# Optimization experiments

Hardware: AMD Instinct MI355X
Metric: run time of the kernel (lower is better)

## Reference

```python
import jax, jax.numpy as jnp
import numpy as np

N_NODES = 50000
N_EDGES = 800000
HDIM = 256
NUMRELS = 16


def setup_inputs() -> dict:
    key = jax.random.key(0)
    ks = jax.random.split(key, 9)
    h = jax.random.normal(ks[0], (N_NODES, HDIM), dtype=jnp.float32)
    relvectors = jax.random.normal(ks[1], (NUMRELS, HDIM), dtype=jnp.float32)
    # GRUCell params (torch layout: [3*hdim, hdim] rows = [r, z, n])
    s = 1.0 / np.sqrt(HDIM)
    w_ih = jax.random.uniform(ks[2], (3 * HDIM, HDIM), minval=-s, maxval=s, dtype=jnp.float32)
    w_hh = jax.random.uniform(ks[3], (3 * HDIM, HDIM), minval=-s, maxval=s, dtype=jnp.float32)
    b_ih = jax.random.uniform(ks[4], (3 * HDIM,), minval=-s, maxval=s, dtype=jnp.float32)
    b_hh = jax.random.uniform(ks[5], (3 * HDIM,), minval=-s, maxval=s, dtype=jnp.float32)
    edge_src = jax.random.randint(ks[6], (N_EDGES,), 0, N_NODES, dtype=jnp.int32)
    edge_dst = jax.random.randint(ks[7], (N_EDGES,), 0, N_NODES, dtype=jnp.int32)
    edge_rel = jax.random.randint(ks[8], (N_EDGES,), 0, NUMRELS, dtype=jnp.int32)
    return {"h": h, "relvectors": relvectors, "w_ih": w_ih, "w_hh": w_hh,
            "b_ih": b_ih, "b_hh": b_hh, "edge_src": edge_src,
            "edge_dst": edge_dst, "edge_rel": edge_rel}


def _gru_cell(x, h, w_ih, w_hh, b_ih, b_hh):
    # torch.nn.GRUCell semantics
    gi = x @ w_ih.T + b_ih  # [N, 3H]
    gh = h @ w_hh.T + b_hh  # [N, 3H]
    i_r, i_z, i_n = jnp.split(gi, 3, axis=-1)
    h_r, h_z, h_n = jnp.split(gh, 3, axis=-1)
    r = jax.nn.sigmoid(i_r + h_r)
    z = jax.nn.sigmoid(i_z + h_z)
    n = jnp.tanh(i_n + r * h_n)
    return (1.0 - z) * n + z * h


def reference(h, relvectors, w_ih, w_hh, b_ih, b_hh, edge_src, edge_dst, edge_rel):
    # message: per-edge gather of source node state + relation vector by edge id
    msg = h[edge_src] + relvectors[edge_rel]          # [E, H]
    # reduce: segment-sum over destination nodes (mailbox sum)
    red = jax.ops.segment_sum(msg, edge_dst, num_segments=h.shape[0])  # [N, H]
    # apply: GRUCell node update (input=red, hidden=h)
    return _gru_cell(red, h, w_ih, w_hh, b_ih, b_hh)
```

## Files before the change

kernel.cpp:

```cpp
#include <hip/hip_runtime.h>

#define H 256

typedef __attribute__((ext_vector_type(8))) short short8;
typedef __attribute__((ext_vector_type(8))) unsigned short ushort8v;
typedef __attribute__((ext_vector_type(16))) float f32x16;

__device__ __forceinline__ ushort f2bf(float f) {
  unsigned u = __float_as_uint(f);
  unsigned r = (u + 0x7fffu + ((u >> 16) & 1u)) >> 16;
  return (ushort)r;
}
__device__ __forceinline__ float bf2f(ushort s) {
  return __uint_as_float(((unsigned)s) << 16);
}


__global__ void k_cvt_h(const float* __restrict__ src, ushort* __restrict__ h16row,
                        ushort* __restrict__ hfm, int nrows) {
  int t = blockIdx.x * blockDim.x + threadIdx.x;
  if (t >= nrows * 32) return;
  const int row = t >> 5, l = t & 31;
  const float4 fa = *(const float4*)&src[(size_t)row * H + l * 8];
  const float4 fb = *(const float4*)&src[(size_t)row * H + l * 8 + 4];
  ushort8v o;
  o[0] = f2bf(fa.x); o[1] = f2bf(fa.y); o[2] = f2bf(fa.z); o[3] = f2bf(fa.w);
  o[4] = f2bf(fb.x); o[5] = f2bf(fb.y); o[6] = f2bf(fb.z); o[7] = f2bf(fb.w);
  *(ushort8v*)&h16row[(size_t)row * H + l * 8] = o;
  const int p = row >> 7, r = row & 127;
  *(ushort8v*)((char*)hfm + (size_t)p * 65536 + (size_t)l * 2048 + r * 16) = o;
}

__global__ void k_cvt_w(const float* __restrict__ w, ushort* __restrict__ wfm, int gbase) {
  int t = blockIdx.x * blockDim.x + threadIdx.x;
  if (t >= 768 * 32) return;
  const int j = t >> 5, l = t & 31;
  const float4 fa = *(const float4*)&w[(size_t)j * H + l * 8];
  const float4 fb = *(const float4*)&w[(size_t)j * H + l * 8 + 4];
  ushort8v o;
  o[0] = f2bf(fa.x); o[1] = f2bf(fa.y); o[2] = f2bf(fa.z); o[3] = f2bf(fa.w);
  o[4] = f2bf(fb.x); o[5] = f2bf(fb.y); o[6] = f2bf(fb.z); o[7] = f2bf(fb.w);
  *(ushort8v*)((char*)wfm + ((size_t)l * 1536 + gbase + j) * 16) = o;
}

__global__ void k_zero(int* cnt, int n) {
  int i = blockIdx.x * blockDim.x + threadIdx.x;
  if (i < n) cnt[i] = 0;
}

__global__ void k_hist(const int* __restrict__ dst, int* __restrict__ cnt, int ne) {
  int e = blockIdx.x * blockDim.x + threadIdx.x;
  if (e < ne) atomicAdd(&cnt[dst[e]], 1);
}

__global__ __launch_bounds__(256) void k_scan1(const int* __restrict__ cnt,
                                               int* __restrict__ bsum, int n) {
  __shared__ int s[256];
  int t = threadIdx.x, i = blockIdx.x * 256 + t;
  int v = (i < n) ? cnt[i] : 0;
  s[t] = v;
  __syncthreads();
  for (int o = 128; o > 0; o >>= 1) {
    if (t < o) s[t] += s[t + o];
    __syncthreads();
  }
  if (t == 0) bsum[blockIdx.x] = s[0];
}

__global__ __launch_bounds__(256) void k_scan2(const int* __restrict__ bsum,
                                               int* __restrict__ bpre, int nb,
                                               int* __restrict__ offs, int n) {
  __shared__ int s[256];
  int t = threadIdx.x;
  int v = (t < nb) ? bsum[t] : 0;
  s[t] = v;
  __syncthreads();
  for (int o = 1; o < 256; o <<= 1) {
    int x = (t >= o) ? s[t - o] : 0;
    __syncthreads();
    s[t] += x;
    __syncthreads();
  }
  if (t < nb) bpre[t] = s[t] - v;
  if (t == 255) offs[n] = s[255];
}

__global__ __launch_bounds__(256) void k_scan3(const int* __restrict__ cnt,
                                               const int* __restrict__ bpre,
                                               int* __restrict__ offs,
                                               int* __restrict__ cursor, int n) {
  __shared__ int s[256];
  int t = threadIdx.x, i = blockIdx.x * 256 + t;
  int v = (i < n) ? cnt[i] : 0;
  s[t] = v;
  __syncthreads();
  for (int o = 1; o < 256; o <<= 1) {
    int x = (t >= o) ? s[t - o] : 0;
    __syncthreads();
    s[t] += x;
    __syncthreads();
  }
  if (i < n) {
    int e = bpre[blockIdx.x] + s[t] - v;
    offs[i] = e;
    cursor[i] = e;
  }
}

__global__ void k_fill(const int* __restrict__ src, const int* __restrict__ dst,
                       const int* __restrict__ rel, int* __restrict__ cursor,
                       int* __restrict__ bucket, int ne) {
  int e = blockIdx.x * blockDim.x + threadIdx.x;
  if (e < ne) {
    int p = atomicAdd(&cursor[dst[e]], 1);
    bucket[p] = src[e] | (rel[e] << 16);
  }
}

__global__ __launch_bounds__(256) void k_gather(const ushort* __restrict__ h16,
                                                const float* __restrict__ relv,
                                                const int* __restrict__ offs,
                                                const int* __restrict__ bucket,
                                                ushort* __restrict__ redfm, int nn) {
  const int hw = threadIdx.x >> 5;
  const int l = threadIdx.x & 31;
  const int node = blockIdx.x * 8 + hw;
  if (node >= nn) return;
  const int beg = offs[node], end = offs[node + 1];
  float acc[8] = {0.f, 0.f, 0.f, 0.f, 0.f, 0.f, 0.f, 0.f};
  int i = beg;
  for (; i + 2 <= end; i += 2) {
    const int p0 = bucket[i], p1 = bucket[i + 1];
    const ushort8v a0 = *(const ushort8v*)&h16[(size_t)(p0 & 0xFFFF) * H + l * 8];
    const ushort8v a1 = *(const ushort8v*)&h16[(size_t)(p1 & 0xFFFF) * H + l * 8];
    const float4 r0a = *(const float4*)&relv[(p0 >> 16) * H + l * 8];
    const float4 r0b = *(const float4*)&relv[(p0 >> 16) * H + l * 8 + 4];
    const float4 r1a = *(const float4*)&relv[(p1 >> 16) * H + l * 8];
    const float4 r1b = *(const float4*)&relv[(p1 >> 16) * H + l * 8 + 4];
    acc[0] += bf2f(a0[0]) + r0a.x + bf2f(a1[0]) + r1a.x;
    acc[1] += bf2f(a0[1]) + r0a.y + bf2f(a1[1]) + r1a.y;
    acc[2] += bf2f(a0[2]) + r0a.z + bf2f(a1[2]) + r1a.z;
    acc[3] += bf2f(a0[3]) + r0a.w + bf2f(a1[3]) + r1a.w;
    acc[4] += bf2f(a0[4]) + r0b.x + bf2f(a1[4]) + r1b.x;
    acc[5] += bf2f(a0[5]) + r0b.y + bf2f(a1[5]) + r1b.y;
    acc[6] += bf2f(a0[6]) + r0b.z + bf2f(a1[6]) + r1b.z;
    acc[7] += bf2f(a0[7]) + r0b.w + bf2f(a1[7]) + r1b.w;
  }
  if (i < end) {
    const int p0 = bucket[i];
    const ushort8v a0 = *(const ushort8v*)&h16[(size_t)(p0 & 0xFFFF) * H + l * 8];
    const float4 r0a = *(const float4*)&relv[(p0 >> 16) * H + l * 8];
    const float4 r0b = *(const float4*)&relv[(p0 >> 16) * H + l * 8 + 4];
    acc[0] += bf2f(a0[0]) + r0a.x;
    acc[1] += bf2f(a0[1]) + r0a.y;
    acc[2] += bf2f(a0[2]) + r0a.z;
    acc[3] += bf2f(a0[3]) + r0a.w;
    acc[4] += bf2f(a0[4]) + r0b.x;
    acc[5] += bf2f(a0[5]) + r0b.y;
    acc[6] += bf2f(a0[6]) + r0b.z;
    acc[7] += bf2f(a0[7]) + r0b.w;
  }
  ushort8v o;
#pragma unroll
  for (int e = 0; e < 8; ++e) o[e] = f2bf(acc[e]);
  const int p = node >> 7, r = node & 127;
  *(ushort8v*)((char*)redfm + (size_t)p * 65536 + (size_t)l * 2048 + r * 16) = o;
}

__global__ __launch_bounds__(512, 2) void k_gru_mfma(
    const ushort* __restrict__ redfm, const ushort* __restrict__ hfm,
    const float* __restrict__ hmat, const ushort* __restrict__ wfm,
    const float* __restrict__ b_ih, const float* __restrict__ b_hh,
    float* __restrict__ out, int nn) {
  __shared__ unsigned char smem[49152];
  const int tid = threadIdx.x;
  const int wid = tid >> 6;
  const int lane = tid & 63;
  const int l31 = lane & 31;
  const int lhi = lane >> 5;
  const int row0 = blockIdx.x * 128;
  const int hcol0 = blockIdx.y * 64;
  const bool is_hh = (wid >= 4);
  const int R0 = ((wid >> 1) & 1) * 64;
  const int C = (wid & 1) * 32;

  const char* amat = (const char*)(is_hh ? hfm : redfm);
  const char* wbase = (const char*)wfm;
  const size_t a_base = (size_t)blockIdx.x * 65536 + (size_t)lhi * 2048 + (size_t)(R0 + l31) * 16;
  const size_t b_base = (size_t)lhi * 24576 + (size_t)((is_hh ? 768 : 0) + hcol0 + C + l31) * 16;

  f32x16 acc[2][3] = {};
#pragma unroll 2
  for (int kb = 0; kb < 8; ++kb) {
#pragma unroll
    for (int kg = 0; kg < 2; ++kg) {
      const size_t ao = a_base + (size_t)(kb * 8192 + kg * 4096);
      const size_t bo = b_base + (size_t)(kb * 4 + kg * 2) * 24576;
      const short8 a0 = *(const short8*)(amat + ao);
      const short8 a1 = *(const short8*)(amat + ao + 512);
      const short8 b0 = *(const short8*)(wbase + bo);
      const short8 b1 = *(const short8*)(wbase + bo + 4096);
      const short8 b2 = *(const short8*)(wbase + bo + 8192);
      acc[0][0] = __builtin_amdgcn_mfma_f32_32x32x16_bf16(a0, b0, acc[0][0], 0, 0, 0);
      acc[0][1] = __builtin_amdgcn_mfma_f32_32x32x16_bf16(a0, b1, acc[0][1], 0, 0, 0);
      acc[0][2] = __builtin_amdgcn_mfma_f32_32x32x16_bf16(a0, b2, acc[0][2], 0, 0, 0);
      acc[1][0] = __builtin_amdgcn_mfma_f32_32x32x16_bf16(a1, b0, acc[1][0], 0, 0, 0);
      acc[1][1] = __builtin_amdgcn_mfma_f32_32x32x16_bf16(a1, b1, acc[1][1], 0, 0, 0);
      acc[1][2] = __builtin_amdgcn_mfma_f32_32x32x16_bf16(a1, b2, acc[1][2], 0, 0, 0);
    }
  }

  if (is_hh) {
    const int ww = wid - 4;
#pragma unroll
    for (int rt = 0; rt < 2; ++rt)
#pragma unroll
      for (int s = 0; s < 3; ++s) {
        ushort tmp[16];
#pragma unroll
        for (int r = 0; r < 16; ++r) tmp[r] = f2bf(acc[rt][s][r]);
        const int so = ww * 12288 + (rt * 3 + s) * 2048 + lane * 32;
        *(ushort8v*)&smem[so] = *(const ushort8v*)&tmp[0];
        *(ushort8v*)&smem[so + 16] = *(const ushort8v*)&tmp[8];
      }
  }
  __syncthreads();

  if (!is_hh) {
    const int hcol = hcol0 + C + l31;
    const float bir = b_ih[hcol], biz = b_ih[256 + hcol], bin = b_ih[512 + hcol];
    const float bhr = b_hh[hcol], bhz = b_hh[256 + hcol], bhn = b_hh[512 + hcol];
#pragma unroll
    for (int rt = 0; rt < 2; ++rt) {
      ushort hr_[16], hz_[16], hn_[16];
      const int so = wid * 12288 + rt * 3 * 2048 + lane * 32;
      *(ushort8v*)&hr_[0] = *(const ushort8v*)&smem[so];
      *(ushort8v*)&hr_[8] = *(const ushort8v*)&smem[so + 16];
      *(ushort8v*)&hz_[0] = *(const ushort8v*)&smem[so + 2048];
      *(ushort8v*)&hz_[8] = *(const ushort8v*)&smem[so + 2048 + 16];
      *(ushort8v*)&hn_[0] = *(const ushort8v*)&smem[so + 4096];
      *(ushort8v*)&hn_[8] = *(const ushort8v*)&smem[so + 4096 + 16];
#pragma unroll
      for (int r = 0; r < 16; ++r) {
        const int rowc = (r & 3) + 8 * (r >> 2) + 4 * lhi;
        const int grow = row0 + R0 + rt * 32 + rowc;
        if (grow < nn) {
          const float ir_ = acc[rt][0][r] + bir;
          const float iz_ = acc[rt][1][r] + biz;
          const float in_ = acc[rt][2][r] + bin;
          const float hr = bf2f(hr_[r]) + bhr;
          const float hz = bf2f(hz_[r]) + bhz;
          const float hn = bf2f(hn_[r]) + bhn;
          const float rg = 1.f / (1.f + __expf(-(ir_ + hr)));
          const float zg = 1.f / (1.f + __expf(-(iz_ + hz)));
          const float ng = tanhf(in_ + rg * hn);
          const float hv = hmat[(size_t)grow * H + hcol];
          out[(size_t)grow * H + hcol] = (1.f - zg) * ng + zg * hv;
        }
      }
    }
  }
}

extern "C" void kernel_launch(void* const* d_in, const int* in_sizes, int n_in,
                              void* d_out, int out_size, void* d_ws, size_t ws_size,
                              hipStream_t stream) {
  const float* h    = (const float*)d_in[0];
  const float* relv = (const float*)d_in[1];
  const float* w_ih = (const float*)d_in[2];
  const float* w_hh = (const float*)d_in[3];
  const float* b_ih = (const float*)d_in[4];
  const float* b_hh = (const float*)d_in[5];
  const int* esrc   = (const int*)d_in[6];
  const int* edst   = (const int*)d_in[7];
  const int* erel   = (const int*)d_in[8];
  float* out = (float*)d_out;
  const int nn = in_sizes[0] / H;
  const int ne = in_sizes[6];
  const int npan = (nn + 127) / 128;
  const int nb = (nn + 255) / 256;

  char* w = (char*)d_ws;
  ushort* redfm  = (ushort*)w;  w += (size_t)npan * 65536;
  ushort* hfm    = (ushort*)w;  w += (size_t)npan * 65536;
  ushort* h16row = (ushort*)w;  w += (size_t)nn * H * 2;
  ushort* wfm    = (ushort*)w;  w += (size_t)32 * 1536 * 16;
  int* cnt    = (int*)w;        w += (size_t)nn * 4;
  int* offs   = (int*)w;        w += (size_t)(nn + 4) * 4;
  int* cursor = (int*)w;        w += (size_t)nn * 4;
  int* bsum   = (int*)w;        w += 256 * 4;
  int* bpre   = (int*)w;        w += 256 * 4;
  int* bucket = (int*)w;

  k_cvt_h<<<(nn * 32 + 255) / 256, 256, 0, stream>>>(h, h16row, hfm, nn);
  k_cvt_w<<<96, 256, 0, stream>>>(w_ih, wfm, 0);
  k_cvt_w<<<96, 256, 0, stream>>>(w_hh, wfm, 768);

  k_zero<<<(nn + 255) / 256, 256, 0, stream>>>(cnt, nn);
  k_hist<<<(ne + 255) / 256, 256, 0, stream>>>(edst, cnt, ne);
  k_scan1<<<nb, 256, 0, stream>>>(cnt, bsum, nn);
  k_scan2<<<1, 256, 0, stream>>>(bsum, bpre, nb, offs, nn);
  k_scan3<<<nb, 256, 0, stream>>>(cnt, bpre, offs, cursor, nn);
  k_fill<<<(ne + 255) / 256, 256, 0, stream>>>(esrc, edst, erel, cursor, bucket, ne);

  k_gather<<<(nn + 7) / 8, 256, 0, stream>>>(h16row, relv, offs, bucket, redfm, nn);

  dim3 grid(npan, 4);
  k_gru_mfma<<<grid, 512, 0, stream>>>(redfm, hfm, h, wfm, b_ih, b_hh, out, nn);
}
```

Measured before the change: 407.4 us.

## Count per-relation edges to factor relation vectors; restructure GRU blocks per row panel

The histogram now counts edges per (destination, relation) pair. The gather kernel then sums only the bf16 source rows and adds the relation contribution as count-weighted relation vectors, which removes the per-edge relvector loads and unrolls the source-row gather by four. The GRU kernel changes from a 2D grid of 512-thread blocks to 256-thread blocks over 64-row panels that loop over all four column groups. It reads the hidden-state blend term from the bf16 feature-major copy instead of the fp32 input. The trade-offs are a 16x larger count array (more zeroing and scan reads) and reduced precision for the blend term.

```diff
diff --git a/kernel.cpp b/kernel.cpp
--- a/kernel.cpp
+++ b/kernel.cpp
@@ -48,16 +48,24 @@
   if (i < n) cnt[i] = 0;
 }
 
-__global__ void k_hist(const int* __restrict__ dst, int* __restrict__ cnt, int ne) {
+__global__ void k_hist(const int* __restrict__ dst, const int* __restrict__ rel,
+                       int* __restrict__ cnt16, int ne) {
   int e = blockIdx.x * blockDim.x + threadIdx.x;
-  if (e < ne) atomicAdd(&cnt[dst[e]], 1);
-}
-
-__global__ __launch_bounds__(256) void k_scan1(const int* __restrict__ cnt,
+  if (e < ne) atomicAdd(&cnt16[dst[e] * 16 + rel[e]], 1);
+}
+
+__device__ __forceinline__ int node_cnt(const int* __restrict__ cnt16, int i) {
+  int s = 0;
+#pragma unroll
+  for (int r = 0; r < 16; ++r) s += cnt16[i * 16 + r];
+  return s;
+}
+
+__global__ __launch_bounds__(256) void k_scan1(const int* __restrict__ cnt16,
                                                int* __restrict__ bsum, int n) {
   __shared__ int s[256];
   int t = threadIdx.x, i = blockIdx.x * 256 + t;
-  int v = (i < n) ? cnt[i] : 0;
+  int v = (i < n) ? node_cnt(cnt16, i) : 0;
   s[t] = v;
   __syncthreads();
   for (int o = 128; o > 0; o >>= 1) {
@@ -85,13 +93,13 @@
   if (t == 255) offs[n] = s[255];
 }
 
-__global__ __launch_bounds__(256) void k_scan3(const int* __restrict__ cnt,
+__global__ __launch_bounds__(256) void k_scan3(const int* __restrict__ cnt16,
                                                const int* __restrict__ bpre,
                                                int* __restrict__ offs,
                                                int* __restrict__ cursor, int n) {
   __shared__ int s[256];
   int t = threadIdx.x, i = blockIdx.x * 256 + t;
-  int v = (i < n) ? cnt[i] : 0;
+  int v = (i < n) ? node_cnt(cnt16, i) : 0;
   s[t] = v;
   __syncthreads();
   for (int o = 1; o < 256; o <<= 1) {
@@ -108,12 +116,11 @@
 }
 
 __global__ void k_fill(const int* __restrict__ src, const int* __restrict__ dst,
-                       const int* __restrict__ rel, int* __restrict__ cursor,
-                       int* __restrict__ bucket, int ne) {
+                       int* __restrict__ cursor, int* __restrict__ bucket, int ne) {
   int e = blockIdx.x * blockDim.x + threadIdx.x;
   if (e < ne) {
     int p = atomicAdd(&cursor[dst[e]], 1);
-    bucket[p] = src[e] | (rel[e] << 16);
+    bucket[p] = src[e];
   }
 }
 
@@ -121,6 +128,7 @@
                                                 const float* __restrict__ relv,
                                                 const int* __restrict__ offs,
                                                 const int* __restrict__ bucket,
+                                                const int* __restrict__ cnt16,
                                                 ushort* __restrict__ redfm, int nn) {
   const int hw = threadIdx.x >> 5;
   const int l = threadIdx.x & 31;
@@ -129,36 +137,29 @@
   const int beg = offs[node], end = offs[node + 1];
   float acc[8] = {0.f, 0.f, 0.f, 0.f, 0.f, 0.f, 0.f, 0.f};
   int i = beg;
-  for (; i + 2 <= end; i += 2) {
-    const int p0 = bucket[i], p1 = bucket[i + 1];
-    const ushort8v a0 = *(const ushort8v*)&h16[(size_t)(p0 & 0xFFFF) * H + l * 8];
-    const ushort8v a1 = *(const ushort8v*)&h16[(size_t)(p1 & 0xFFFF) * H + l * 8];
-    const float4 r0a = *(const float4*)&relv[(p0 >> 16) * H + l * 8];
-    const float4 r0b = *(const float4*)&relv[(p0 >> 16) * H + l * 8 + 4];
-    const float4 r1a = *(const float4*)&relv[(p1 >> 16) * H + l * 8];
-    const float4 r1b = *(const float4*)&relv[(p1 >> 16) * H + l * 8 + 4];
-    acc[0] += bf2f(a0[0]) + r0a.x + bf2f(a1[0]) + r1a.x;
-    acc[1] += bf2f(a0[1]) + r0a.y + bf2f(a1[1]) + r1a.y;
-    acc[2] += bf2f(a0[2]) + r0a.z + bf2f(a1[2]) + r1a.z;
-    acc[3] += bf2f(a0[3]) + r0a.w + bf2f(a1[3]) + r1a.w;
-    acc[4] += bf2f(a0[4]) + r0b.x + bf2f(a1[4]) + r1b.x;
-    acc[5] += bf2f(a0[5]) + r0b.y + bf2f(a1[5]) + r1b.y;
-    acc[6] += bf2f(a0[6]) + r0b.z + bf2f(a1[6]) + r1b.z;
-    acc[7] += bf2f(a0[7]) + r0b.w + bf2f(a1[7]) + r1b.w;
-  }
-  if (i < end) {
-    const int p0 = bucket[i];
-    const ushort8v a0 = *(const ushort8v*)&h16[(size_t)(p0 & 0xFFFF) * H + l * 8];
-    const float4 r0a = *(const float4*)&relv[(p0 >> 16) * H + l * 8];
-    const float4 r0b = *(const float4*)&relv[(p0 >> 16) * H + l * 8 + 4];
-    acc[0] += bf2f(a0[0]) + r0a.x;
-    acc[1] += bf2f(a0[1]) + r0a.y;
-    acc[2] += bf2f(a0[2]) + r0a.z;
-    acc[3] += bf2f(a0[3]) + r0a.w;
-    acc[4] += bf2f(a0[4]) + r0b.x;
-    acc[5] += bf2f(a0[5]) + r0b.y;
-    acc[6] += bf2f(a0[6]) + r0b.z;
-    acc[7] += bf2f(a0[7]) + r0b.w;
+  for (; i + 4 <= end; i += 4) {
+    const int s0 = bucket[i], s1 = bucket[i + 1], s2 = bucket[i + 2], s3 = bucket[i + 3];
+    const ushort8v a0 = *(const ushort8v*)&h16[(size_t)s0 * H + l * 8];
+    const ushort8v a1 = *(const ushort8v*)&h16[(size_t)s1 * H + l * 8];
+    const ushort8v a2 = *(const ushort8v*)&h16[(size_t)s2 * H + l * 8];
+    const ushort8v a3 = *(const ushort8v*)&h16[(size_t)s3 * H + l * 8];
+#pragma unroll
+    for (int e = 0; e < 8; ++e)
+      acc[e] += (bf2f(a0[e]) + bf2f(a1[e])) + (bf2f(a2[e]) + bf2f(a3[e]));
+  }
+  for (; i < end; ++i) {
+    const int s0 = bucket[i];
+    const ushort8v a0 = *(const ushort8v*)&h16[(size_t)s0 * H + l * 8];
+#pragma unroll
+    for (int e = 0; e < 8; ++e) acc[e] += bf2f(a0[e]);
+  }
+#pragma unroll 4
+  for (int r = 0; r < 16; ++r) {
+    const float cf = (float)cnt16[node * 16 + r];
+    const float4 ra = *(const float4*)&relv[r * H + l * 8];
+    const float4 rb = *(const float4*)&relv[r * H + l * 8 + 4];
+    acc[0] += cf * ra.x; acc[1] += cf * ra.y; acc[2] += cf * ra.z; acc[3] += cf * ra.w;
+    acc[4] += cf * rb.x; acc[5] += cf * rb.y; acc[6] += cf * rb.z; acc[7] += cf * rb.w;
   }
   ushort8v o;
 #pragma unroll
@@ -167,98 +168,105 @@
   *(ushort8v*)((char*)redfm + (size_t)p * 65536 + (size_t)l * 2048 + r * 16) = o;
 }
 
-__global__ __launch_bounds__(512, 2) void k_gru_mfma(
+__global__ __launch_bounds__(256, 3) void k_gru_mfma(
     const ushort* __restrict__ redfm, const ushort* __restrict__ hfm,
-    const float* __restrict__ hmat, const ushort* __restrict__ wfm,
+    const ushort* __restrict__ wfm,
     const float* __restrict__ b_ih, const float* __restrict__ b_hh,
     float* __restrict__ out, int nn) {
-  __shared__ unsigned char smem[49152];
+  __shared__ unsigned char smem[24576];
   const int tid = threadIdx.x;
   const int wid = tid >> 6;
   const int lane = tid & 63;
   const int l31 = lane & 31;
   const int lhi = lane >> 5;
-  const int row0 = blockIdx.x * 128;
-  const int hcol0 = blockIdx.y * 64;
-  const bool is_hh = (wid >= 4);
-  const int R0 = ((wid >> 1) & 1) * 64;
+  const bool is_hh = (wid >= 2);
   const int C = (wid & 1) * 32;
+  const int row0 = blockIdx.x * 64;
+  const int p = blockIdx.x >> 1;
+  const int rbase = (blockIdx.x & 1) * 64;
 
   const char* amat = (const char*)(is_hh ? hfm : redfm);
-  const char* wbase = (const char*)wfm;
-  const size_t a_base = (size_t)blockIdx.x * 65536 + (size_t)lhi * 2048 + (size_t)(R0 + l31) * 16;
-  const size_t b_base = (size_t)lhi * 24576 + (size_t)((is_hh ? 768 : 0) + hcol0 + C + l31) * 16;
-
-  f32x16 acc[2][3] = {};
-#pragma unroll 2
-  for (int kb = 0; kb < 8; ++kb) {
-#pragma unroll
-    for (int kg = 0; kg < 2; ++kg) {
-      const size_t ao = a_base + (size_t)(kb * 8192 + kg * 4096);
-      const size_t bo = b_base + (size_t)(kb * 4 + kg * 2) * 24576;
-      const short8 a0 = *(const short8*)(amat + ao);
-      const short8 a1 = *(const short8*)(amat + ao + 512);
-      const short8 b0 = *(const short8*)(wbase + bo);
-      const short8 b1 = *(const short8*)(wbase + bo + 4096);
-      const short8 b2 = *(const short8*)(wbase + bo + 8192);
-      acc[0][0] = __builtin_amdgcn_mfma_f32_32x32x16_bf16(a0, b0, acc[0][0], 0, 0, 0);
-      acc[0][1] = __builtin_amdgcn_mfma_f32_32x32x16_bf16(a0, b1, acc[0][1], 0, 0, 0);
-      acc[0][2] = __builtin_amdgcn_mfma_f32_32x32x16_bf16(a0, b2, acc[0][2], 0, 0, 0);
-      acc[1][0] = __builtin_amdgcn_mfma_f32_32x32x16_bf16(a1, b0, acc[1][0], 0, 0, 0);
-      acc[1][1] = __builtin_amdgcn_mfma_f32_32x32x16_bf16(a1, b1, acc[1][1], 0, 0, 0);
-      acc[1][2] = __builtin_amdgcn_mfma_f32_32x32x16_bf16(a1, b2, acc[1][2], 0, 0, 0);
+  const char* wb = (const char*)wfm;
+  const char* hchar = (const char*)hfm;
+  const int a_base = p * 65536 + lhi * 2048 + (rbase + l31) * 16;
+  const int gsel = is_hh ? 768 : 0;
+
+  for (int cw = 0; cw < 4; ++cw) {
+    const int hcol0 = cw * 64;
+    const int b_base = lhi * 24576 + (gsel + hcol0 + C + l31) * 16;
+    f32x16 acc[2][3] = {};
+#pragma unroll
+    for (int kb = 0; kb < 8; ++kb) {
+#pragma unroll
+      for (int kg = 0; kg < 2; ++kg) {
+        const int ao = a_base + kb * 8192 + kg * 4096;
+        const int bo = b_base + (kb * 4 + kg * 2) * 24576;
+        const short8 a0 = *(const short8*)(amat + ao);
+        const short8 a1 = *(const short8*)(amat + ao + 512);
+        const short8 b0 = *(const short8*)(wb + bo);
+        const short8 b1 = *(const short8*)(wb + bo + 4096);
+        const short8 b2 = *(const short8*)(wb + bo + 8192);
+        acc[0][0] = __builtin_amdgcn_mfma_f32_32x32x16_bf16(a0, b0, acc[0][0], 0, 0, 0);
+        acc[0][1] = __builtin_amdgcn_mfma_f32_32x32x16_bf16(a0, b1, acc[0][1], 0, 0, 0);
+        acc[0][2] = __builtin_amdgcn_mfma_f32_32x32x16_bf16(a0, b2, acc[0][2], 0, 0, 0);
+        acc[1][0] = __builtin_amdgcn_mfma_f32_32x32x16_bf16(a1, b0, acc[1][0], 0, 0, 0);
+        acc[1][1] = __builtin_amdgcn_mfma_f32_32x32x16_bf16(a1, b1, acc[1][1], 0, 0, 0);
+        acc[1][2] = __builtin_amdgcn_mfma_f32_32x32x16_bf16(a1, b2, acc[1][2], 0, 0, 0);
+      }
     }
-  }
-
-  if (is_hh) {
-    const int ww = wid - 4;
-#pragma unroll
-    for (int rt = 0; rt < 2; ++rt)
-#pragma unroll
-      for (int s = 0; s < 3; ++s) {
-        ushort tmp[16];
-#pragma unroll
-        for (int r = 0; r < 16; ++r) tmp[r] = f2bf(acc[rt][s][r]);
-        const int so = ww * 12288 + (rt * 3 + s) * 2048 + lane * 32;
-        *(ushort8v*)&smem[so] = *(const ushort8v*)&tmp[0];
-        *(ushort8v*)&smem[so + 16] = *(const ushort8v*)&tmp[8];
-      }
-  }
-  __syncthreads();
-
-  if (!is_hh) {
-    const int hcol = hcol0 + C + l31;
-    const float bir = b_ih[hcol], biz = b_ih[256 + hcol], bin = b_ih[512 + hcol];
-    const float bhr = b_hh[hcol], bhz = b_hh[256 + hcol], bhn = b_hh[512 + hcol];
-#pragma unroll
-    for (int rt = 0; rt < 2; ++rt) {
-      ushort hr_[16], hz_[16], hn_[16];
-      const int so = wid * 12288 + rt * 3 * 2048 + lane * 32;
-      *(ushort8v*)&hr_[0] = *(const ushort8v*)&smem[so];
-      *(ushort8v*)&hr_[8] = *(const ushort8v*)&smem[so + 16];
-      *(ushort8v*)&hz_[0] = *(const ushort8v*)&smem[so + 2048];
-      *(ushort8v*)&hz_[8] = *(const ushort8v*)&smem[so + 2048 + 16];
-      *(ushort8v*)&hn_[0] = *(const ushort8v*)&smem[so + 4096];
-      *(ushort8v*)&hn_[8] = *(const ushort8v*)&smem[so + 4096 + 16];
-#pragma unroll
-      for (int r = 0; r < 16; ++r) {
-        const int rowc = (r & 3) + 8 * (r >> 2) + 4 * lhi;
-        const int grow = row0 + R0 + rt * 32 + rowc;
-        if (grow < nn) {
-          const float ir_ = acc[rt][0][r] + bir;
-          const float iz_ = acc[rt][1][r] + biz;
-          const float in_ = acc[rt][2][r] + bin;
-          const float hr = bf2f(hr_[r]) + bhr;
-          const float hz = bf2f(hz_[r]) + bhz;
-          const float hn = bf2f(hn_[r]) + bhn;
-          const float rg = 1.f / (1.f + __expf(-(ir_ + hr)));
-          const float zg = 1.f / (1.f + __expf(-(iz_ + hz)));
-          const float ng = tanhf(in_ + rg * hn);
-          const float hv = hmat[(size_t)grow * H + hcol];
-          out[(size_t)grow * H + hcol] = (1.f - zg) * ng + zg * hv;
+
+    if (is_hh) {
+      const int ww = wid - 2;
+#pragma unroll
+      for (int rt = 0; rt < 2; ++rt)
+#pragma unroll
+        for (int s = 0; s < 3; ++s) {
+          ushort tmp[16];
+#pragma unroll
+          for (int r = 0; r < 16; ++r) tmp[r] = f2bf(acc[rt][s][r]);
+          const int so = ww * 12288 + (rt * 3 + s) * 2048 + lane * 32;
+          *(ushort8v*)&smem[so] = *(const ushort8v*)&tmp[0];
+          *(ushort8v*)&smem[so + 16] = *(const ushort8v*)&tmp[8];
+        }
+    }
+    __syncthreads();
+
+    if (!is_hh) {
+      const int hcol = hcol0 + C + l31;
+      const float bir = b_ih[hcol], biz = b_ih[256 + hcol], bin = b_ih[512 + hcol];
+      const float bhr = b_hh[hcol], bhz = b_hh[256 + hcol], bhn = b_hh[512 + hcol];
+      const int hv_base = p * 65536 + (hcol >> 3) * 2048 + (hcol & 7) * 2;
+#pragma unroll
+      for (int rt = 0; rt < 2; ++rt) {
+        ushort hr_[16], hz_[16], hn_[16];
+        const int so = wid * 12288 + rt * 3 * 2048 + lane * 32;
+        *(ushort8v*)&hr_[0] = *(const ushort8v*)&smem[so];
+        *(ushort8v*)&hr_[8] = *(const ushort8v*)&smem[so + 16];
+        *(ushort8v*)&hz_[0] = *(const ushort8v*)&smem[so + 2048];
+        *(ushort8v*)&hz_[8] = *(const ushort8v*)&smem[so + 2048 + 16];
+        *(ushort8v*)&hn_[0] = *(const ushort8v*)&smem[so + 4096];
+        *(ushort8v*)&hn_[8] = *(const ushort8v*)&smem[so + 4096 + 16];
+#pragma unroll
+        for (int r = 0; r < 16; ++r) {
+          const int rowc = (r & 3) + 8 * (r >> 2) + 4 * lhi;
+          const int grow = row0 + rt * 32 + rowc;
+          if (grow < nn) {
+            const float ir_ = acc[rt][0][r] + bir;
+            const float iz_ = acc[rt][1][r] + biz;
+            const float in_ = acc[rt][2][r] + bin;
+            const float hr = bf2f(hr_[r]) + bhr;
+            const float hz = bf2f(hz_[r]) + bhz;
+            const float hn = bf2f(hn_[r]) + bhn;
+            const float rg = 1.f / (1.f + __expf(-(ir_ + hr)));
+            const float zg = 1.f / (1.f + __expf(-(iz_ + hz)));
+            const float ng = tanhf(in_ + rg * hn);
+            const float hv = bf2f(*(const ushort*)(hchar + hv_base + (rbase + rt * 32 + rowc) * 16));
+            out[(size_t)grow * H + hcol] = (1.f - zg) * ng + zg * hv;
+          }
         }
       }
     }
+    __syncthreads();
   }
 }
 
@@ -285,7 +293,7 @@
   ushort* hfm    = (ushort*)w;  w += (size_t)npan * 65536;
   ushort* h16row = (ushort*)w;  w += (size_t)nn * H * 2;
   ushort* wfm    = (ushort*)w;  w += (size_t)32 * 1536 * 16;
-  int* cnt    = (int*)w;        w += (size_t)nn * 4;
+  int* cnt16  = (int*)w;        w += (size_t)nn * 16 * 4;
   int* offs   = (int*)w;        w += (size_t)(nn + 4) * 4;
   int* cursor = (int*)w;        w += (size_t)nn * 4;
   int* bsum   = (int*)w;        w += 256 * 4;
@@ -296,15 +304,14 @@
   k_cvt_w<<<96, 256, 0, stream>>>(w_ih, wfm, 0);
   k_cvt_w<<<96, 256, 0, stream>>>(w_hh, wfm, 768);
 
-  k_zero<<<(nn + 255) / 256, 256, 0, stream>>>(cnt, nn);
-  k_hist<<<(ne + 255) / 256, 256, 0, stream>>>(edst, cnt, ne);
-  k_scan1<<<nb, 256, 0, stream>>>(cnt, bsum, nn);
+  k_zero<<<(nn * 16 + 255) / 256, 256, 0, stream>>>(cnt16, nn * 16);
+  k_hist<<<(ne + 255) / 256, 256, 0, stream>>>(edst, erel, cnt16, ne);
+  k_scan1<<<nb, 256, 0, stream>>>(cnt16, bsum, nn);
   k_scan2<<<1, 256, 0, stream>>>(bsum, bpre, nb, offs, nn);
-  k_scan3<<<nb, 256, 0, stream>>>(cnt, bpre, offs, cursor, nn);
-  k_fill<<<(ne + 255) / 256, 256, 0, stream>>>(esrc, edst, erel, cursor, bucket, ne);
-
-  k_gather<<<(nn + 7) / 8, 256, 0, stream>>>(h16row, relv, offs, bucket, redfm, nn);
-
-  dim3 grid(npan, 4);
-  k_gru_mfma<<<grid, 512, 0, stream>>>(redfm, hfm, h, wfm, b_ih, b_hh, out, nn);
-}
+  k_scan3<<<nb, 256, 0, stream>>>(cnt16, bpre, offs, cursor, nn);
+  k_fill<<<(ne + 255) / 256, 256, 0, stream>>>(esrc, edst, cursor, bucket, ne);
+
+  k_gather<<<(nn + 7) / 8, 256, 0, stream>>>(h16row, relv, offs, bucket, cnt16, redfm, nn);
+
+  k_gru_mfma<<<782, 256, 0, stream>>>(redfm, hfm, wfm, b_ih, b_hh, out, nn);
+}
```

Measured after the change: 528.4 us. 29.7% more time.
